# Optimization experiments

Measured on AMD Instinct MI355X. Metric: run time of the kernel, lower is better.

## Reference

```python
import jax, jax.numpy as jnp
import numpy as np

B, S, HID = 2, 2048, 2048
NH, NKV = 16, 4
HD = HID // NH  # 128
GROUPS = NH // NKV


def _rope(x, cos, sin):
    # x: [B, S, H, D]; cos/sin: [S, D//2]
    xr = x.reshape(*x.shape[:-1], HD // 2, 2)
    x0, x1 = xr[..., 0], xr[..., 1]
    c = cos[None, :, None, :]
    s = sin[None, :, None, :]
    o0 = x0 * c - x1 * s
    o1 = x0 * s + x1 * c
    return jnp.stack([o0, o1], axis=-1).reshape(*x.shape)


def setup_inputs() -> dict:
    key = jax.random.key(0)
    k1, k2, k3, k4, k5, k6 = jax.random.split(key, 6)
    hidden_states = jax.random.normal(k1, (B, S, HID), dtype=jnp.float32)
    # RoPE frequencies (llama-style)
    inv_freq = 1.0 / (10000.0 ** (np.arange(0, HD, 2, dtype=np.float32) / HD))
    t = np.arange(S, dtype=np.float32)
    ang = np.outer(t, inv_freq)  # [S, HD//2]
    freqs_cos = jnp.asarray(np.cos(ang), dtype=jnp.float32)
    freqs_sin = jnp.asarray(np.sin(ang), dtype=jnp.float32)
    # additive causal mask [1,1,S,S]
    causal = jnp.triu(jnp.full((S, S), -1e9, dtype=jnp.float32), k=1)
    attention_mask = causal[None, None]
    sc = 0.02
    Wq = jax.random.normal(k2, (NH * HD, HID), dtype=jnp.float32) * sc
    Wk = jax.random.normal(k3, (NKV * HD, HID), dtype=jnp.float32) * sc
    Wv = jax.random.normal(k4, (NKV * HD, HID), dtype=jnp.float32) * sc
    Wo = jax.random.normal(k5, (HID, NH * HD), dtype=jnp.float32) * sc
    return {"hidden_states": hidden_states, "freqs_cos": freqs_cos,
            "freqs_sin": freqs_sin, "attention_mask": attention_mask,
            "Wq": Wq, "Wk": Wk, "Wv": Wv, "Wo": Wo}


def reference(hidden_states, freqs_cos, freqs_sin, attention_mask, Wq, Wk, Wv, Wo):
    xq = (hidden_states @ Wq.T).reshape(B, S, NH, HD)
    xk = (hidden_states @ Wk.T).reshape(B, S, NKV, HD)
    xv = (hidden_states @ Wv.T).reshape(B, S, NKV, HD)
    xq = _rope(xq, freqs_cos, freqs_sin)
    xk = _rope(xk, freqs_cos, freqs_sin)
    # expand KV heads for GQA: [B,S,NKV,D] -> [B,S,NH,D]
    xk = jnp.repeat(xk, GROUPS, axis=2)
    xv = jnp.repeat(xv, GROUPS, axis=2)
    q = xq.transpose(0, 2, 1, 3)  # [B,H,S,D]
    k = xk.transpose(0, 2, 1, 3)
    v = xv.transpose(0, 2, 1, 3)
    scores = jnp.einsum('bhqd,bhkd->bhqk', q, k) / jnp.sqrt(jnp.float32(HD))
    scores = scores + attention_mask
    probs = jax.nn.softmax(scores, axis=-1)
    out = jnp.einsum('bhqk,bhkd->bhqd', probs, v)
    out = out.transpose(0, 2, 1, 3).reshape(B, S, NH * HD)
    return out @ Wo.T
```

## Files before the change

kernel.cpp:

```cpp
#include <hip/hip_runtime.h>


typedef __attribute__((ext_vector_type(8))) short bf16x8;
typedef __attribute__((ext_vector_type(4))) float f32x4;
typedef __attribute__((ext_vector_type(16))) float f32x16;
typedef __attribute__((ext_vector_type(4))) unsigned short u16x4;
typedef unsigned short u16;

#define B_   2
#define S_   2048
#define HID_ 2048
#define NH_  16
#define NKV_ 4
#define HD_  128

__device__ __forceinline__ u16 f2bf(float f) {
  unsigned u = __float_as_uint(f);
  u = (u + 0x7FFFu + ((u >> 16) & 1u)) >> 16;
  return (u16)u;
}
__device__ __forceinline__ float bf2f(u16 h) {
  return __uint_as_float(((unsigned)h) << 16);
}

__device__ __forceinline__ void gl_lds16(const void* g, void* l) {
  __builtin_amdgcn_global_load_lds(
      (const __attribute__((address_space(1))) void*)g,
      (__attribute__((address_space(3))) void*)l, 16, 0, 0);
}

__global__ void convert_bf16(const float* __restrict__ src, u16* __restrict__ dst, int n8) {
  int i = blockIdx.x * 256 + threadIdx.x;
  if (i >= n8) return;
  const float4* s = (const float4*)src + (size_t)i * 2;
  float4 a = s[0], b = s[1];
  union { u16 u[8]; uint4 v; } o;
  o.u[0] = f2bf(a.x); o.u[1] = f2bf(a.y); o.u[2] = f2bf(a.z); o.u[3] = f2bf(a.w);
  o.u[4] = f2bf(b.x); o.u[5] = f2bf(b.y); o.u[6] = f2bf(b.z); o.u[7] = f2bf(b.w);
  ((uint4*)dst)[i] = o.v;
}

template<int EPI>
__launch_bounds__(256, 2)
__global__ void gemm128(const u16* __restrict__ A, const u16* __restrict__ Bm,
                        float* __restrict__ C, u16* __restrict__ Qb,
                        u16* __restrict__ Kb, u16* __restrict__ Vb,
                        int N, int K)
{
  __shared__ u16 As[128 * 64];
  __shared__ u16 Bs[128 * 64];
  const int tid = threadIdx.x;
  const int lane = tid & 63;
  const int w = tid >> 6;
  const int lo = lane & 15, hi = lane >> 4;
  const int wr = w >> 1, wc = w & 1;
  const int rowA0 = blockIdx.x * 128;
  const int rowB0 = blockIdx.y * 128;

  f32x4 acc[4][4] = {};

  for (int kt = 0; kt < K; kt += 64) {
    __syncthreads();
#pragma unroll
    for (int it = 0; it < 4; ++it) {
      int c = it * 256 + tid;
      int r = c >> 3;
      int cb = (c & 7) * 8;
      gl_lds16(A + (size_t)(rowA0 + r) * K + kt + cb, (char*)As + c * 16);
      gl_lds16(Bm + (size_t)(rowB0 + r) * K + kt + cb, (char*)Bs + c * 16);
    }
    __syncthreads();
#pragma unroll
    for (int kk = 0; kk < 64; kk += 32) {
      bf16x8 af[4], bfr[4];
#pragma unroll
      for (int m = 0; m < 4; ++m)
        af[m] = *(const bf16x8*)(As + (wr * 64 + m * 16 + lo) * 64 + kk + hi * 8);
#pragma unroll
      for (int n = 0; n < 4; ++n)
        bfr[n] = *(const bf16x8*)(Bs + (wc * 64 + n * 16 + lo) * 64 + kk + hi * 8);
#pragma unroll
      for (int m = 0; m < 4; ++m)
#pragma unroll
        for (int n = 0; n < 4; ++n)
          acc[m][n] = __builtin_amdgcn_mfma_f32_16x16x32_bf16(af[m], bfr[n], acc[m][n], 0, 0, 0);
    }
  }

#pragma unroll
  for (int m = 0; m < 4; ++m) {
#pragma unroll
    for (int n = 0; n < 4; ++n) {
#pragma unroll
      for (int r = 0; r < 4; ++r) {
        int grow = rowA0 + wr * 64 + m * 16 + hi * 4 + r;
        int gcol = rowB0 + wc * 64 + n * 16 + lo;
        float v = acc[m][n][r];
        if (EPI == 0) {
          C[(size_t)grow * N + gcol] = v;
        } else {
          int bb = grow >> 11, s = grow & 2047;
          u16 hv = f2bf(v);
          if (gcol < 2048) {
            int h = gcol >> 7, d = gcol & 127;
            Qb[(((size_t)bb * NH_ + h) * S_ + s) * HD_ + d] = hv;
          } else if (gcol < 2560) {
            int h = (gcol - 2048) >> 7, d = gcol & 127;
            Kb[(((size_t)bb * NKV_ + h) * S_ + s) * HD_ + d] = hv;
          } else {
            int h = (gcol - 2560) >> 7, d = gcol & 127;
            Vb[(((size_t)bb * NKV_ + h) * S_ + s) * HD_ + d] = hv;
          }
        }
      }
    }
  }
}

__global__ void rope_k(u16* __restrict__ Qb, u16* __restrict__ Kb,
                       const float* __restrict__ fcos, const float* __restrict__ fsin)
{
  int idx = blockIdx.x * 256 + threadIdx.x;
  int chunk = idx & 15;
  int s = (idx >> 4) & 2047;
  int hs = idx >> 15;
  u16* p = (hs < 32) ? (Qb + ((size_t)hs * S_ + s) * HD_ + chunk * 8)
                     : (Kb + ((size_t)(hs - 32) * S_ + s) * HD_ + chunk * 8);
  uint4 raw = *(uint4*)p;
  float4 c4 = *(const float4*)(fcos + (size_t)s * 64 + chunk * 4);
  float4 s4 = *(const float4*)(fsin + (size_t)s * 64 + chunk * 4);
  float cc[4] = {c4.x, c4.y, c4.z, c4.w};
  float ss[4] = {s4.x, s4.y, s4.z, s4.w};
  unsigned* rw = (unsigned*)&raw;
#pragma unroll
  for (int j = 0; j < 4; ++j) {
    float x0 = bf2f((u16)(rw[j] & 0xFFFFu));
    float x1 = bf2f((u16)(rw[j] >> 16));
    float o0 = x0 * cc[j] - x1 * ss[j];
    float o1 = x0 * ss[j] + x1 * cc[j];
    rw[j] = (unsigned)f2bf(o0) | ((unsigned)f2bf(o1) << 16);
  }
  *(uint4*)p = raw;
}

__global__ void transpose_v(const u16* __restrict__ Vb, u16* __restrict__ Vtg)
{
  __shared__ u16 t[64][65];
  const int st = blockIdx.x, dt = blockIdx.y, hs = blockIdx.z;
  const u16* src = Vb + ((size_t)hs * S_ + st * 64) * HD_ + dt * 64;
#pragma unroll
  for (int it = 0; it < 2; ++it) {
    int c = it * 256 + threadIdx.x;
    int r = c >> 3, cb = (c & 7) * 8;
    uint4 v = *(const uint4*)(src + (size_t)r * HD_ + cb);
    u16* u = (u16*)&v;
#pragma unroll
    for (int e = 0; e < 8; ++e) t[r][cb + e] = u[e];
  }
  __syncthreads();
#pragma unroll
  for (int it = 0; it < 2; ++it) {
    int c = it * 256 + threadIdx.x;
    int r2 = c >> 3, cb2 = (c & 7) * 8;
    union { u16 u[8]; uint4 v; } o;
#pragma unroll
    for (int e = 0; e < 8; ++e) o.u[e] = t[cb2 + e][r2];
    *(uint4*)(Vtg + ((size_t)hs * HD_ + dt * 64 + r2) * S_ + st * 64 + cb2) = o.v;
  }
}

__launch_bounds__(128, 2)
__global__ void flash_attn(const u16* __restrict__ Qb, const u16* __restrict__ Kb,
                           const u16* __restrict__ Vtg, u16* __restrict__ AO)
{
  __shared__ u16 Ks[2][64 * 128];
  __shared__ u16 Vt[2][128 * 64];

  const int tid = threadIdx.x, lane = tid & 63, w = tid >> 6;
  const int ql = lane & 31, hh = lane >> 5;
  const int swl = (ql & 7) ^ ((ql >> 3) & 3);
  const int h = blockIdx.y, b = blockIdx.z, kvh = h >> 2;
  const u16* Qh = Qb + ((size_t)b * NH_ + h) * S_ * HD_;
  const u16* Kh = Kb + ((size_t)b * NKV_ + kvh) * S_ * HD_;
  const u16* Vh = Vtg + ((size_t)b * NKV_ + kvh) * HD_ * S_;
  const float cf = 0.12752704581383682f;
  const float NEG = -30000.f;

  auto STAGE = [&](int buf, int kt) {
#pragma unroll
    for (int it = 0; it < 8; ++it) {
      int c = it * 128 + tid;
      int r = c >> 4;
      int slot = (c & 15) ^ (r & 7) ^ ((r >> 3) & 3);
      gl_lds16(Kh + (size_t)(kt + r) * HD_ + slot * 8, (char*)Ks[buf] + c * 16);
    }
#pragma unroll
    for (int it = 0; it < 8; ++it) {
      int c = it * 128 + tid;
      int r = c >> 3;
      int slot = (c & 7) ^ ((r & 7) ^ ((r >> 3) & 3));
      gl_lds16(Vh + (size_t)r * S_ + kt + slot * 8, (char*)Vt[buf] + c * 16);
    }
  };

  for (int pass = 0; pass < 2; ++pass) {
    const int qb = pass ? (31 - (int)blockIdx.x) : (int)blockIdx.x;
    const int q0w = qb * 64 + w * 32;
    const int qg = q0w + ql;
    const int nt = qb + 1;

    bf16x8 qf[8];
#pragma unroll
    for (int s = 0; s < 8; ++s)
      qf[s] = *(const bf16x8*)(Qh + (size_t)qg * HD_ + s * 16 + hh * 8);

    f32x16 o[4] = {};
    float m = NEG, l = 0.f;

    __syncthreads();
    STAGE(0, 0);
    __syncthreads();
    int cur = 0;

    for (int t = 0; t < nt; ++t) {
      if (t < nt - 1) STAGE(cur ^ 1, (t + 1) * 64);
      const int kt = t * 64;
      if (kt < q0w + 32) {
        f32x16 st[2] = {};
        __builtin_amdgcn_s_setprio(1);
#pragma unroll
        for (int sl = 0; sl < 8; ++sl) {
          int slot = ((2 * sl + hh) ^ swl) * 16;
          bf16x8 k0 = *(const bf16x8*)((const char*)Ks[cur] + ql * 256 + slot);
          bf16x8 k1 = *(const bf16x8*)((const char*)Ks[cur] + (32 + ql) * 256 + slot);
          st[0] = __builtin_amdgcn_mfma_f32_32x32x16_bf16(k0, qf[sl], st[0], 0, 0, 0);
          st[1] = __builtin_amdgcn_mfma_f32_32x32x16_bf16(k1, qf[sl], st[1], 0, 0, 0);
        }
        __builtin_amdgcn_s_setprio(0);

        if ((kt + 63) > q0w) {
#pragma unroll
          for (int i = 0; i < 2; ++i)
#pragma unroll
            for (int r = 0; r < 16; ++r) {
              int kv = kt + 32 * i + (r & 3) + 8 * (r >> 2) + 4 * hh;
              if (kv > qg) st[i][r] = NEG;
            }
        }

        float mx[8];
#pragma unroll
        for (int r = 0; r < 8; ++r)
          mx[r] = fmaxf(fmaxf(st[0][r], st[0][r + 8]), fmaxf(st[1][r], st[1][r + 8]));
#pragma unroll
        for (int d = 4; d > 0; d >>= 1)
#pragma unroll
          for (int r = 0; r < d; ++r) mx[r] = fmaxf(mx[r], mx[r + d]);
        float tmax = fmaxf(mx[0], __shfl_xor(mx[0], 32));

        float mn = fmaxf(m, tmax);
        float rs = __builtin_exp2f((m - mn) * cf);
        m = mn; l *= rs;
#pragma unroll
        for (int dt = 0; dt < 4; ++dt)
#pragma unroll
          for (int r = 0; r < 16; ++r) o[dt][r] *= rs;

        const float mc = m * cf;
#pragma unroll
        for (int i = 0; i < 2; ++i)
#pragma unroll
          for (int r = 0; r < 16; ++r)
            st[i][r] = __builtin_exp2f(__builtin_fmaf(st[i][r], cf, -mc));
        float sm[8];
#pragma unroll
        for (int r = 0; r < 8; ++r)
          sm[r] = (st[0][r] + st[0][r + 8]) + (st[1][r] + st[1][r + 8]);
#pragma unroll
        for (int d = 4; d > 0; d >>= 1)
#pragma unroll
          for (int r = 0; r < d; ++r) sm[r] += sm[r + d];
        l += sm[0] + __shfl_xor(sm[0], 32);

        bf16x8 pb[4];
#pragma unroll
        for (int i = 0; i < 2; ++i)
#pragma unroll
          for (int s = 0; s < 2; ++s) {
            unsigned wA, wC, wB, wD;
            asm("v_cvt_pk_bf16_f32 %0, %1, %2" : "=v"(wA) : "v"(st[i][8*s+0]), "v"(st[i][8*s+1]));
            asm("v_cvt_pk_bf16_f32 %0, %1, %2" : "=v"(wC) : "v"(st[i][8*s+2]), "v"(st[i][8*s+3]));
            asm("v_cvt_pk_bf16_f32 %0, %1, %2" : "=v"(wB) : "v"(st[i][8*s+4]), "v"(st[i][8*s+5]));
            asm("v_cvt_pk_bf16_f32 %0, %1, %2" : "=v"(wD) : "v"(st[i][8*s+6]), "v"(st[i][8*s+7]));
            unsigned tA = (unsigned)__shfl_xor((int)wA, 32);
            unsigned tB = (unsigned)__shfl_xor((int)wB, 32);
            unsigned tC = (unsigned)__shfl_xor((int)wC, 32);
            unsigned tD = (unsigned)__shfl_xor((int)wD, 32);
            union { unsigned u[4]; bf16x8 v; } pk;
            pk.u[0] = hh ? tB : wA;
            pk.u[1] = hh ? tD : wC;
            pk.u[2] = hh ? wB : tA;
            pk.u[3] = hh ? wD : tC;
            pb[2 * i + s] = pk.v;
          }

        __builtin_amdgcn_s_setprio(1);
#pragma unroll
        for (int dt = 0; dt < 4; ++dt)
#pragma unroll
          for (int ks = 0; ks < 4; ++ks) {
            int row = 32 * dt + ql;
            bf16x8 vf = *(const bf16x8*)((const char*)Vt[cur] + row * 128 +
                                         (((2 * ks + hh) ^ swl) & 7) * 16);
            o[dt] = __builtin_amdgcn_mfma_f32_32x32x16_bf16(vf, pb[ks], o[dt], 0, 0, 0);
          }
        __builtin_amdgcn_s_setprio(0);
      }
      __syncthreads();
      cur ^= 1;
    }

    const float inv = 1.f / l;
#pragma unroll
    for (int dt = 0; dt < 4; ++dt)
#pragma unroll
      for (int g = 0; g < 4; ++g) {
        u16x4 pk4;
#pragma unroll
        for (int e = 0; e < 4; ++e) pk4[e] = f2bf(o[dt][4 * g + e] * inv);
        *(u16x4*)(AO + ((size_t)b * S_ + qg) * HID_ + h * HD_ + 32 * dt + 8 * g + 4 * hh) = pk4;
      }
  }
}

extern "C" void kernel_launch(void* const* d_in, const int* in_sizes, int n_in,
                              void* d_out, int out_size, void* d_ws, size_t ws_size,
                              hipStream_t stream)
{
  (void)in_sizes; (void)n_in; (void)out_size; (void)ws_size;
  const float* X  = (const float*)d_in[0];
  const float* fc = (const float*)d_in[1];
  const float* fs = (const float*)d_in[2];
  const float* Wq = (const float*)d_in[4];
  const float* Wk = (const float*)d_in[5];
  const float* Wv = (const float*)d_in[6];
  const float* Wo = (const float*)d_in[7];
  float* out = (float*)d_out;

  u16* Xb  = (u16*)d_ws;
  u16* Wb  = Xb + (size_t)4096 * 2048;
  u16* Qb  = Wb + (size_t)3072 * 2048;
  u16* Kb  = Qb + (size_t)B_ * NH_ * S_ * HD_;
  u16* Vb  = Kb + (size_t)B_ * NKV_ * S_ * HD_;
  u16* AO  = Xb;
  u16* Wob = Wb;
  u16* Vtg = Wb + (size_t)2048 * 2048;

  convert_bf16<<<4096, 256, 0, stream>>>(X,  Xb,               4096 * 2048 / 8);
  convert_bf16<<<2048, 256, 0, stream>>>(Wq, Wb,               2048 * 2048 / 8);
  convert_bf16<<<512,  256, 0, stream>>>(Wk, Wb + 2048 * 2048, 512 * 2048 / 8);
  convert_bf16<<<512,  256, 0, stream>>>(Wv, Wb + 2560 * 2048, 512 * 2048 / 8);

  gemm128<1><<<dim3(32, 24), 256, 0, stream>>>(Xb, Wb, nullptr, Qb, Kb, Vb, 3072, 2048);

  convert_bf16<<<2048, 256, 0, stream>>>(Wo, Wob, 2048 * 2048 / 8);

  transpose_v<<<dim3(32, 2, 8), 256, 0, stream>>>(Vb, Vtg);

  rope_k<<<5120, 256, 0, stream>>>(Qb, Kb, fc, fs);

  flash_attn<<<dim3(16, NH_, B_), 128, 0, stream>>>(Qb, Kb, Vtg, AO);

  gemm128<0><<<dim3(32, 16), 256, 0, stream>>>(AO, Wob, out, nullptr, nullptr, nullptr, 2048, 2048);
}
```

Before: 240.2 us.

## Drop LDS staging in flash attention; waves load K/V directly from global

Flash attention no longer uses double-buffered shared-memory tiles and barriers. Each of four waves per block takes its own 32-row query tile, chosen so causal work balances across waves, and loads K and V fragments straight from global memory into registers before the MFMAs. A lazy rescale skips the accumulator correction when the running max grows by only a small amount. This removes LDS traffic and block syncs at the cost of redundant global/L2 loads of K and V across waves, and more register pressure.

```diff
diff --git a/kernel.cpp b/kernel.cpp
--- a/kernel.cpp
+++ b/kernel.cpp
@@ -169,168 +169,144 @@
   }
 }
 
-__launch_bounds__(128, 2)
+__launch_bounds__(256, 2)
 __global__ void flash_attn(const u16* __restrict__ Qb, const u16* __restrict__ Kb,
                            const u16* __restrict__ Vtg, u16* __restrict__ AO)
 {
-  __shared__ u16 Ks[2][64 * 128];
-  __shared__ u16 Vt[2][128 * 64];
-
   const int tid = threadIdx.x, lane = tid & 63, w = tid >> 6;
   const int ql = lane & 31, hh = lane >> 5;
-  const int swl = (ql & 7) ^ ((ql >> 3) & 3);
-  const int h = blockIdx.y, b = blockIdx.z, kvh = h >> 2;
+  const int x = blockIdx.x, h = blockIdx.y, b = blockIdx.z, kvh = h >> 2;
   const u16* Qh = Qb + ((size_t)b * NH_ + h) * S_ * HD_;
   const u16* Kh = Kb + ((size_t)b * NKV_ + kvh) * S_ * HD_;
   const u16* Vh = Vtg + ((size_t)b * NKV_ + kvh) * HD_ * S_;
   const float cf = 0.12752704581383682f;
   const float NEG = -30000.f;
 
-  auto STAGE = [&](int buf, int kt) {
-#pragma unroll
-    for (int it = 0; it < 8; ++it) {
-      int c = it * 128 + tid;
-      int r = c >> 4;
-      int slot = (c & 15) ^ (r & 7) ^ ((r >> 3) & 3);
-      gl_lds16(Kh + (size_t)(kt + r) * HD_ + slot * 8, (char*)Ks[buf] + c * 16);
-    }
-#pragma unroll
-    for (int it = 0; it < 8; ++it) {
-      int c = it * 128 + tid;
-      int r = c >> 3;
-      int slot = (c & 7) ^ ((r & 7) ^ ((r >> 3) & 3));
-      gl_lds16(Vh + (size_t)r * S_ + kt + slot * 8, (char*)Vt[buf] + c * 16);
-    }
-  };
-
-  for (int pass = 0; pass < 2; ++pass) {
-    const int qb = pass ? (31 - (int)blockIdx.x) : (int)blockIdx.x;
-    const int q0w = qb * 64 + w * 32;
-    const int qg = q0w + ql;
-    const int nt = qb + 1;
-
-    bf16x8 qf[8];
-#pragma unroll
-    for (int s = 0; s < 8; ++s)
-      qf[s] = *(const bf16x8*)(Qh + (size_t)qg * HD_ + s * 16 + hh * 8);
-
-    f32x16 o[4] = {};
-    float m = NEG, l = 0.f;
-
-    __syncthreads();
-    STAGE(0, 0);
-    __syncthreads();
-    int cur = 0;
-
-    for (int t = 0; t < nt; ++t) {
-      if (t < nt - 1) STAGE(cur ^ 1, (t + 1) * 64);
-      const int kt = t * 64;
-      if (kt < q0w + 32) {
-        f32x16 st[2] = {};
-        __builtin_amdgcn_s_setprio(1);
-#pragma unroll
-        for (int sl = 0; sl < 8; ++sl) {
-          int slot = ((2 * sl + hh) ^ swl) * 16;
-          bf16x8 k0 = *(const bf16x8*)((const char*)Ks[cur] + ql * 256 + slot);
-          bf16x8 k1 = *(const bf16x8*)((const char*)Ks[cur] + (32 + ql) * 256 + slot);
-          st[0] = __builtin_amdgcn_mfma_f32_32x32x16_bf16(k0, qf[sl], st[0], 0, 0, 0);
-          st[1] = __builtin_amdgcn_mfma_f32_32x32x16_bf16(k1, qf[sl], st[1], 0, 0, 0);
+  const int qt = (w == 0) ? x : (w == 1) ? (63 - x) : (w == 2) ? (31 - x) : (32 + x);
+  const int q0 = qt * 32;
+  const int qg = q0 + ql;
+  const int nt = (qt >> 1) + 1;
+
+  bf16x8 qf[8];
+#pragma unroll
+  for (int s = 0; s < 8; ++s)
+    qf[s] = *(const bf16x8*)(Qh + (size_t)qg * HD_ + s * 16 + hh * 8);
+
+  f32x16 o[4] = {};
+  float m = NEG, l = 0.f;
+
+  for (int t = 0; t < nt; ++t) {
+    const int kt = t * 64;
+    const u16* Kt = Kh + (size_t)kt * HD_;
+
+    bf16x8 k0[8], k1[8];
+#pragma unroll
+    for (int sl = 0; sl < 8; ++sl)
+      k0[sl] = *(const bf16x8*)(Kt + (size_t)ql * HD_ + sl * 16 + hh * 8);
+#pragma unroll
+    for (int sl = 0; sl < 8; ++sl)
+      k1[sl] = *(const bf16x8*)(Kt + (size_t)(32 + ql) * HD_ + sl * 16 + hh * 8);
+    f32x16 st[2] = {};
+    __builtin_amdgcn_s_setprio(1);
+#pragma unroll
+    for (int sl = 0; sl < 8; ++sl) {
+      st[0] = __builtin_amdgcn_mfma_f32_32x32x16_bf16(k0[sl], qf[sl], st[0], 0, 0, 0);
+      st[1] = __builtin_amdgcn_mfma_f32_32x32x16_bf16(k1[sl], qf[sl], st[1], 0, 0, 0);
+    }
+    __builtin_amdgcn_s_setprio(0);
+
+    if (kt + 63 > q0) {
+#pragma unroll
+      for (int i = 0; i < 2; ++i)
+#pragma unroll
+        for (int r = 0; r < 16; ++r) {
+          int kv = kt + 32 * i + (r & 3) + 8 * (r >> 2) + 4 * hh;
+          if (kv > qg) st[i][r] = NEG;
         }
-        __builtin_amdgcn_s_setprio(0);
-
-        if ((kt + 63) > q0w) {
-#pragma unroll
-          for (int i = 0; i < 2; ++i)
-#pragma unroll
-            for (int r = 0; r < 16; ++r) {
-              int kv = kt + 32 * i + (r & 3) + 8 * (r >> 2) + 4 * hh;
-              if (kv > qg) st[i][r] = NEG;
-            }
-        }
-
-        float mx[8];
-#pragma unroll
-        for (int r = 0; r < 8; ++r)
-          mx[r] = fmaxf(fmaxf(st[0][r], st[0][r + 8]), fmaxf(st[1][r], st[1][r + 8]));
-#pragma unroll
-        for (int d = 4; d > 0; d >>= 1)
-#pragma unroll
-          for (int r = 0; r < d; ++r) mx[r] = fmaxf(mx[r], mx[r + d]);
-        float tmax = fmaxf(mx[0], __shfl_xor(mx[0], 32));
-
-        float mn = fmaxf(m, tmax);
-        float rs = __builtin_exp2f((m - mn) * cf);
-        m = mn; l *= rs;
-#pragma unroll
-        for (int dt = 0; dt < 4; ++dt)
-#pragma unroll
-          for (int r = 0; r < 16; ++r) o[dt][r] *= rs;
-
-        const float mc = m * cf;
-#pragma unroll
-        for (int i = 0; i < 2; ++i)
-#pragma unroll
-          for (int r = 0; r < 16; ++r)
-            st[i][r] = __builtin_exp2f(__builtin_fmaf(st[i][r], cf, -mc));
-        float sm[8];
-#pragma unroll
-        for (int r = 0; r < 8; ++r)
-          sm[r] = (st[0][r] + st[0][r + 8]) + (st[1][r] + st[1][r + 8]);
-#pragma unroll
-        for (int d = 4; d > 0; d >>= 1)
-#pragma unroll
-          for (int r = 0; r < d; ++r) sm[r] += sm[r + d];
-        l += sm[0] + __shfl_xor(sm[0], 32);
-
-        bf16x8 pb[4];
-#pragma unroll
-        for (int i = 0; i < 2; ++i)
-#pragma unroll
-          for (int s = 0; s < 2; ++s) {
-            unsigned wA, wC, wB, wD;
-            asm("v_cvt_pk_bf16_f32 %0, %1, %2" : "=v"(wA) : "v"(st[i][8*s+0]), "v"(st[i][8*s+1]));
-            asm("v_cvt_pk_bf16_f32 %0, %1, %2" : "=v"(wC) : "v"(st[i][8*s+2]), "v"(st[i][8*s+3]));
-            asm("v_cvt_pk_bf16_f32 %0, %1, %2" : "=v"(wB) : "v"(st[i][8*s+4]), "v"(st[i][8*s+5]));
-            asm("v_cvt_pk_bf16_f32 %0, %1, %2" : "=v"(wD) : "v"(st[i][8*s+6]), "v"(st[i][8*s+7]));
-            unsigned tA = (unsigned)__shfl_xor((int)wA, 32);
-            unsigned tB = (unsigned)__shfl_xor((int)wB, 32);
-            unsigned tC = (unsigned)__shfl_xor((int)wC, 32);
-            unsigned tD = (unsigned)__shfl_xor((int)wD, 32);
-            union { unsigned u[4]; bf16x8 v; } pk;
-            pk.u[0] = hh ? tB : wA;
-            pk.u[1] = hh ? tD : wC;
-            pk.u[2] = hh ? wB : tA;
-            pk.u[3] = hh ? wD : tC;
-            pb[2 * i + s] = pk.v;
-          }
-
-        __builtin_amdgcn_s_setprio(1);
-#pragma unroll
-        for (int dt = 0; dt < 4; ++dt)
-#pragma unroll
-          for (int ks = 0; ks < 4; ++ks) {
-            int row = 32 * dt + ql;
-            bf16x8 vf = *(const bf16x8*)((const char*)Vt[cur] + row * 128 +
-                                         (((2 * ks + hh) ^ swl) & 7) * 16);
-            o[dt] = __builtin_amdgcn_mfma_f32_32x32x16_bf16(vf, pb[ks], o[dt], 0, 0, 0);
-          }
-        __builtin_amdgcn_s_setprio(0);
+    }
+
+    float mx[8];
+#pragma unroll
+    for (int r = 0; r < 8; ++r)
+      mx[r] = fmaxf(fmaxf(st[0][r], st[0][r + 8]), fmaxf(st[1][r], st[1][r + 8]));
+#pragma unroll
+    for (int d = 4; d > 0; d >>= 1)
+#pragma unroll
+      for (int r = 0; r < d; ++r) mx[r] = fmaxf(mx[r], mx[r + d]);
+    float tmax = fmaxf(mx[0], __shfl_xor(mx[0], 32));
+
+    if (!__all((tmax - m) * cf <= 8.f)) {
+      float mn = fmaxf(m, tmax);
+      float rs = __builtin_exp2f((m - mn) * cf);
+      m = mn; l *= rs;
+#pragma unroll
+      for (int dt = 0; dt < 4; ++dt)
+#pragma unroll
+        for (int r = 0; r < 16; ++r) o[dt][r] *= rs;
+    }
+
+    const float mc = m * cf;
+#pragma unroll
+    for (int i = 0; i < 2; ++i)
+#pragma unroll
+      for (int r = 0; r < 16; ++r)
+        st[i][r] = __builtin_exp2f(__builtin_fmaf(st[i][r], cf, -mc));
+    float sm[8];
+#pragma unroll
+    for (int r = 0; r < 8; ++r)
+      sm[r] = (st[0][r] + st[0][r + 8]) + (st[1][r] + st[1][r + 8]);
+#pragma unroll
+    for (int d = 4; d > 0; d >>= 1)
+#pragma unroll
+      for (int r = 0; r < d; ++r) sm[r] += sm[r + d];
+    l += sm[0] + __shfl_xor(sm[0], 32);
+
+    bf16x8 pb[4];
+#pragma unroll
+    for (int i = 0; i < 2; ++i)
+#pragma unroll
+      for (int s = 0; s < 2; ++s) {
+        unsigned wA, wC, wB, wD;
+        asm("v_cvt_pk_bf16_f32 %0, %1, %2" : "=v"(wA) : "v"(st[i][8*s+0]), "v"(st[i][8*s+1]));
+        asm("v_cvt_pk_bf16_f32 %0, %1, %2" : "=v"(wC) : "v"(st[i][8*s+2]), "v"(st[i][8*s+3]));
+        asm("v_cvt_pk_bf16_f32 %0, %1, %2" : "=v"(wB) : "v"(st[i][8*s+4]), "v"(st[i][8*s+5]));
+        asm("v_cvt_pk_bf16_f32 %0, %1, %2" : "=v"(wD) : "v"(st[i][8*s+6]), "v"(st[i][8*s+7]));
+        unsigned tA = (unsigned)__shfl_xor((int)wA, 32);
+        unsigned tB = (unsigned)__shfl_xor((int)wB, 32);
+        unsigned tC = (unsigned)__shfl_xor((int)wC, 32);
+        unsigned tD = (unsigned)__shfl_xor((int)wD, 32);
+        union { unsigned u[4]; bf16x8 v; } pk;
+        pk.u[0] = hh ? tB : wA;
+        pk.u[1] = hh ? tD : wC;
+        pk.u[2] = hh ? wB : tA;
+        pk.u[3] = hh ? wD : tC;
+        pb[2 * i + s] = pk.v;
       }
-      __syncthreads();
-      cur ^= 1;
-    }
-
-    const float inv = 1.f / l;
-#pragma unroll
-    for (int dt = 0; dt < 4; ++dt)
-#pragma unroll
-      for (int g = 0; g < 4; ++g) {
-        u16x4 pk4;
-#pragma unroll
-        for (int e = 0; e < 4; ++e) pk4[e] = f2bf(o[dt][4 * g + e] * inv);
-        *(u16x4*)(AO + ((size_t)b * S_ + qg) * HID_ + h * HD_ + 32 * dt + 8 * g + 4 * hh) = pk4;
-      }
-  }
+
+#pragma unroll
+    for (int dt = 0; dt < 4; ++dt) {
+      bf16x8 vf[4];
+#pragma unroll
+      for (int ks = 0; ks < 4; ++ks)
+        vf[ks] = *(const bf16x8*)(Vh + (size_t)(32 * dt + ql) * S_ + kt + ks * 16 + hh * 8);
+      __builtin_amdgcn_s_setprio(1);
+#pragma unroll
+      for (int ks = 0; ks < 4; ++ks)
+        o[dt] = __builtin_amdgcn_mfma_f32_32x32x16_bf16(vf[ks], pb[ks], o[dt], 0, 0, 0);
+      __builtin_amdgcn_s_setprio(0);
+    }
+  }
+
+  const float inv = 1.f / l;
+#pragma unroll
+  for (int dt = 0; dt < 4; ++dt)
+#pragma unroll
+    for (int g = 0; g < 4; ++g) {
+      u16x4 pk4;
+#pragma unroll
+      for (int e = 0; e < 4; ++e) pk4[e] = f2bf(o[dt][4 * g + e] * inv);
+      *(u16x4*)(AO + ((size_t)b * S_ + qg) * HID_ + h * HD_ + 32 * dt + 8 * g + 4 * hh) = pk4;
+    }
 }
 
 extern "C" void kernel_launch(void* const* d_in, const int* in_sizes, int n_in,
@@ -369,7 +345,7 @@
 
   rope_k<<<5120, 256, 0, stream>>>(Qb, Kb, fc, fs);
 
-  flash_attn<<<dim3(16, NH_, B_), 128, 0, stream>>>(Qb, Kb, Vtg, AO);
+  flash_attn<<<dim3(16, NH_, B_), 256, 0, stream>>>(Qb, Kb, Vtg, AO);
 
   gemm128<0><<<dim3(32, 16), 256, 0, stream>>>(AO, Wob, out, nullptr, nullptr, nullptr, 2048, 2048);
 }
```

Measured after the change: 289.8 us. 20.6% more time.

## Restructure flash attention into 4-wave blocks with balanced causal tiles and lazy rescale

Applied to the files above, without the earlier changes.

Replaces the two-pass, two-wave flash attention block with a single-pass, four-wave block. Each wave takes a 32-row query tile chosen from a complementary set (x, 63-x, 31-x, 32+x), so each block carries a similar amount of causal work and one staged K/V pipeline is shared by more waves. The grid is flattened, and the block index is mapped so that blocks sharing a KV head and batch sit close together, which should help L2 reuse. It also adds a lazy softmax rescale that skips the max update and the accumulator rescale while the new maximum stays within a bounded exponent, trading fewer VALU multiplies for extra range reliance on fp32 accumulation.

```diff
diff --git a/kernel.cpp b/kernel.cpp
--- a/kernel.cpp
+++ b/kernel.cpp
@@ -169,7 +169,7 @@
   }
 }
 
-__launch_bounds__(128, 2)
+__launch_bounds__(256, 2)
 __global__ void flash_attn(const u16* __restrict__ Qb, const u16* __restrict__ Kb,
                            const u16* __restrict__ Vtg, u16* __restrict__ AO)
 {
@@ -179,85 +179,90 @@
   const int tid = threadIdx.x, lane = tid & 63, w = tid >> 6;
   const int ql = lane & 31, hh = lane >> 5;
   const int swl = (ql & 7) ^ ((ql >> 3) & 3);
-  const int h = blockIdx.y, b = blockIdx.z, kvh = h >> 2;
+
+  const int lin = blockIdx.x;
+  const int g = lin & 7, idx = lin >> 3;
+  const int b = g >> 2, kvh = g & 3;
+  const int h = kvh * 4 + (idx >> 4);
+  const int x = idx & 15;
+
   const u16* Qh = Qb + ((size_t)b * NH_ + h) * S_ * HD_;
   const u16* Kh = Kb + ((size_t)b * NKV_ + kvh) * S_ * HD_;
   const u16* Vh = Vtg + ((size_t)b * NKV_ + kvh) * HD_ * S_;
   const float cf = 0.12752704581383682f;
   const float NEG = -30000.f;
 
+  const int qt = (w == 0) ? x : (w == 1) ? (63 - x) : (w == 2) ? (31 - x) : (32 + x);
+  const int q0 = qt * 32;
+  const int qg = q0 + ql;
+  const int bnt = ((63 - x) >> 1) + 1;
+
   auto STAGE = [&](int buf, int kt) {
 #pragma unroll
-    for (int it = 0; it < 8; ++it) {
-      int c = it * 128 + tid;
+    for (int it = 0; it < 4; ++it) {
+      int c = it * 256 + tid;
       int r = c >> 4;
       int slot = (c & 15) ^ (r & 7) ^ ((r >> 3) & 3);
       gl_lds16(Kh + (size_t)(kt + r) * HD_ + slot * 8, (char*)Ks[buf] + c * 16);
     }
 #pragma unroll
-    for (int it = 0; it < 8; ++it) {
-      int c = it * 128 + tid;
+    for (int it = 0; it < 4; ++it) {
+      int c = it * 256 + tid;
       int r = c >> 3;
       int slot = (c & 7) ^ ((r & 7) ^ ((r >> 3) & 3));
       gl_lds16(Vh + (size_t)r * S_ + kt + slot * 8, (char*)Vt[buf] + c * 16);
     }
   };
 
-  for (int pass = 0; pass < 2; ++pass) {
-    const int qb = pass ? (31 - (int)blockIdx.x) : (int)blockIdx.x;
-    const int q0w = qb * 64 + w * 32;
-    const int qg = q0w + ql;
-    const int nt = qb + 1;
-
-    bf16x8 qf[8];
-#pragma unroll
-    for (int s = 0; s < 8; ++s)
-      qf[s] = *(const bf16x8*)(Qh + (size_t)qg * HD_ + s * 16 + hh * 8);
-
-    f32x16 o[4] = {};
-    float m = NEG, l = 0.f;
-
-    __syncthreads();
-    STAGE(0, 0);
-    __syncthreads();
-    int cur = 0;
-
-    for (int t = 0; t < nt; ++t) {
-      if (t < nt - 1) STAGE(cur ^ 1, (t + 1) * 64);
-      const int kt = t * 64;
-      if (kt < q0w + 32) {
-        f32x16 st[2] = {};
-        __builtin_amdgcn_s_setprio(1);
-#pragma unroll
-        for (int sl = 0; sl < 8; ++sl) {
-          int slot = ((2 * sl + hh) ^ swl) * 16;
-          bf16x8 k0 = *(const bf16x8*)((const char*)Ks[cur] + ql * 256 + slot);
-          bf16x8 k1 = *(const bf16x8*)((const char*)Ks[cur] + (32 + ql) * 256 + slot);
-          st[0] = __builtin_amdgcn_mfma_f32_32x32x16_bf16(k0, qf[sl], st[0], 0, 0, 0);
-          st[1] = __builtin_amdgcn_mfma_f32_32x32x16_bf16(k1, qf[sl], st[1], 0, 0, 0);
-        }
-        __builtin_amdgcn_s_setprio(0);
-
-        if ((kt + 63) > q0w) {
-#pragma unroll
-          for (int i = 0; i < 2; ++i)
-#pragma unroll
-            for (int r = 0; r < 16; ++r) {
-              int kv = kt + 32 * i + (r & 3) + 8 * (r >> 2) + 4 * hh;
-              if (kv > qg) st[i][r] = NEG;
-            }
-        }
-
-        float mx[8];
-#pragma unroll
-        for (int r = 0; r < 8; ++r)
-          mx[r] = fmaxf(fmaxf(st[0][r], st[0][r + 8]), fmaxf(st[1][r], st[1][r + 8]));
-#pragma unroll
-        for (int d = 4; d > 0; d >>= 1)
-#pragma unroll
-          for (int r = 0; r < d; ++r) mx[r] = fmaxf(mx[r], mx[r + d]);
-        float tmax = fmaxf(mx[0], __shfl_xor(mx[0], 32));
-
+  bf16x8 qf[8];
+#pragma unroll
+  for (int s = 0; s < 8; ++s)
+    qf[s] = *(const bf16x8*)(Qh + (size_t)qg * HD_ + s * 16 + hh * 8);
+
+  f32x16 o[4] = {};
+  float m = NEG, l = 0.f;
+
+  STAGE(0, 0);
+  __syncthreads();
+  int cur = 0;
+
+  for (int t = 0; t < bnt; ++t) {
+    if (t + 1 < bnt) STAGE(cur ^ 1, (t + 1) * 64);
+    const int kt = t * 64;
+    if (kt < q0 + 32) {
+      f32x16 st[2] = {};
+      __builtin_amdgcn_s_setprio(1);
+#pragma unroll
+      for (int sl = 0; sl < 8; ++sl) {
+        int slot = ((2 * sl + hh) ^ swl) * 16;
+        bf16x8 k0 = *(const bf16x8*)((const char*)Ks[cur] + ql * 256 + slot);
+        bf16x8 k1 = *(const bf16x8*)((const char*)Ks[cur] + (32 + ql) * 256 + slot);
+        st[0] = __builtin_amdgcn_mfma_f32_32x32x16_bf16(k0, qf[sl], st[0], 0, 0, 0);
+        st[1] = __builtin_amdgcn_mfma_f32_32x32x16_bf16(k1, qf[sl], st[1], 0, 0, 0);
+      }
+      __builtin_amdgcn_s_setprio(0);
+
+      if ((kt + 63) > q0) {
+#pragma unroll
+        for (int i = 0; i < 2; ++i)
+#pragma unroll
+          for (int r = 0; r < 16; ++r) {
+            int kv = kt + 32 * i + (r & 3) + 8 * (r >> 2) + 4 * hh;
+            if (kv > qg) st[i][r] = NEG;
+          }
+      }
+
+      float mx[8];
+#pragma unroll
+      for (int r = 0; r < 8; ++r)
+        mx[r] = fmaxf(fmaxf(st[0][r], st[0][r + 8]), fmaxf(st[1][r], st[1][r + 8]));
+#pragma unroll
+      for (int d = 4; d > 0; d >>= 1)
+#pragma unroll
+        for (int r = 0; r < d; ++r) mx[r] = fmaxf(mx[r], mx[r + d]);
+      float tmax = fmaxf(mx[0], __shfl_xor(mx[0], 32));
+
+      if (!__all((tmax - m) * cf <= 8.f)) {
         float mn = fmaxf(m, tmax);
         float rs = __builtin_exp2f((m - mn) * cf);
         m = mn; l *= rs;
@@ -265,72 +270,72 @@
         for (int dt = 0; dt < 4; ++dt)
 #pragma unroll
           for (int r = 0; r < 16; ++r) o[dt][r] *= rs;
-
-        const float mc = m * cf;
-#pragma unroll
-        for (int i = 0; i < 2; ++i)
-#pragma unroll
-          for (int r = 0; r < 16; ++r)
-            st[i][r] = __builtin_exp2f(__builtin_fmaf(st[i][r], cf, -mc));
-        float sm[8];
-#pragma unroll
-        for (int r = 0; r < 8; ++r)
-          sm[r] = (st[0][r] + st[0][r + 8]) + (st[1][r] + st[1][r + 8]);
-#pragma unroll
-        for (int d = 4; d > 0; d >>= 1)
-#pragma unroll
-          for (int r = 0; r < d; ++r) sm[r] += sm[r + d];
-        l += sm[0] + __shfl_xor(sm[0], 32);
-
-        bf16x8 pb[4];
-#pragma unroll
-        for (int i = 0; i < 2; ++i)
-#pragma unroll
-          for (int s = 0; s < 2; ++s) {
-            unsigned wA, wC, wB, wD;
-            asm("v_cvt_pk_bf16_f32 %0, %1, %2" : "=v"(wA) : "v"(st[i][8*s+0]), "v"(st[i][8*s+1]));
-            asm("v_cvt_pk_bf16_f32 %0, %1, %2" : "=v"(wC) : "v"(st[i][8*s+2]), "v"(st[i][8*s+3]));
-            asm("v_cvt_pk_bf16_f32 %0, %1, %2" : "=v"(wB) : "v"(st[i][8*s+4]), "v"(st[i][8*s+5]));
-            asm("v_cvt_pk_bf16_f32 %0, %1, %2" : "=v"(wD) : "v"(st[i][8*s+6]), "v"(st[i][8*s+7]));
-            unsigned tA = (unsigned)__shfl_xor((int)wA, 32);
-            unsigned tB = (unsigned)__shfl_xor((int)wB, 32);
-            unsigned tC = (unsigned)__shfl_xor((int)wC, 32);
-            unsigned tD = (unsigned)__shfl_xor((int)wD, 32);
-            union { unsigned u[4]; bf16x8 v; } pk;
-            pk.u[0] = hh ? tB : wA;
-            pk.u[1] = hh ? tD : wC;
-            pk.u[2] = hh ? wB : tA;
-            pk.u[3] = hh ? wD : tC;
-            pb[2 * i + s] = pk.v;
-          }
-
-        __builtin_amdgcn_s_setprio(1);
-#pragma unroll
-        for (int dt = 0; dt < 4; ++dt)
-#pragma unroll
-          for (int ks = 0; ks < 4; ++ks) {
-            int row = 32 * dt + ql;
-            bf16x8 vf = *(const bf16x8*)((const char*)Vt[cur] + row * 128 +
-                                         (((2 * ks + hh) ^ swl) & 7) * 16);
-            o[dt] = __builtin_amdgcn_mfma_f32_32x32x16_bf16(vf, pb[ks], o[dt], 0, 0, 0);
-          }
-        __builtin_amdgcn_s_setprio(0);
       }
-      __syncthreads();
-      cur ^= 1;
-    }
-
-    const float inv = 1.f / l;
-#pragma unroll
-    for (int dt = 0; dt < 4; ++dt)
-#pragma unroll
-      for (int g = 0; g < 4; ++g) {
-        u16x4 pk4;
-#pragma unroll
-        for (int e = 0; e < 4; ++e) pk4[e] = f2bf(o[dt][4 * g + e] * inv);
-        *(u16x4*)(AO + ((size_t)b * S_ + qg) * HID_ + h * HD_ + 32 * dt + 8 * g + 4 * hh) = pk4;
-      }
-  }
+
+      const float mc = m * cf;
+#pragma unroll
+      for (int i = 0; i < 2; ++i)
+#pragma unroll
+        for (int r = 0; r < 16; ++r)
+          st[i][r] = __builtin_exp2f(__builtin_fmaf(st[i][r], cf, -mc));
+      float sm[8];
+#pragma unroll
+      for (int r = 0; r < 8; ++r)
+        sm[r] = (st[0][r] + st[0][r + 8]) + (st[1][r] + st[1][r + 8]);
+#pragma unroll
+      for (int d = 4; d > 0; d >>= 1)
+#pragma unroll
+        for (int r = 0; r < d; ++r) sm[r] += sm[r + d];
+      l += sm[0] + __shfl_xor(sm[0], 32);
+
+      bf16x8 pb[4];
+#pragma unroll
+      for (int i = 0; i < 2; ++i)
+#pragma unroll
+        for (int s = 0; s < 2; ++s) {
+          unsigned wA, wC, wB, wD;
+          asm("v_cvt_pk_bf16_f32 %0, %1, %2" : "=v"(wA) : "v"(st[i][8*s+0]), "v"(st[i][8*s+1]));
+          asm("v_cvt_pk_bf16_f32 %0, %1, %2" : "=v"(wC) : "v"(st[i][8*s+2]), "v"(st[i][8*s+3]));
+          asm("v_cvt_pk_bf16_f32 %0, %1, %2" : "=v"(wB) : "v"(st[i][8*s+4]), "v"(st[i][8*s+5]));
+          asm("v_cvt_pk_bf16_f32 %0, %1, %2" : "=v"(wD) : "v"(st[i][8*s+6]), "v"(st[i][8*s+7]));
+          unsigned tA = (unsigned)__shfl_xor((int)wA, 32);
+          unsigned tB = (unsigned)__shfl_xor((int)wB, 32);
+          unsigned tC = (unsigned)__shfl_xor((int)wC, 32);
+          unsigned tD = (unsigned)__shfl_xor((int)wD, 32);
+          union { unsigned u[4]; bf16x8 v; } pk;
+          pk.u[0] = hh ? tB : wA;
+          pk.u[1] = hh ? tD : wC;
+          pk.u[2] = hh ? wB : tA;
+          pk.u[3] = hh ? wD : tC;
+          pb[2 * i + s] = pk.v;
+        }
+
+      __builtin_amdgcn_s_setprio(1);
+#pragma unroll
+      for (int dt = 0; dt < 4; ++dt)
+#pragma unroll
+        for (int ks = 0; ks < 4; ++ks) {
+          int row = 32 * dt + ql;
+          bf16x8 vf = *(const bf16x8*)((const char*)Vt[cur] + row * 128 +
+                                       (((2 * ks + hh) ^ swl) & 7) * 16);
+          o[dt] = __builtin_amdgcn_mfma_f32_32x32x16_bf16(vf, pb[ks], o[dt], 0, 0, 0);
+        }
+      __builtin_amdgcn_s_setprio(0);
+    }
+    __syncthreads();
+    cur ^= 1;
+  }
+
+  const float inv = 1.f / l;
+#pragma unroll
+  for (int dt = 0; dt < 4; ++dt)
+#pragma unroll
+    for (int gi = 0; gi < 4; ++gi) {
+      u16x4 pk4;
+#pragma unroll
+      for (int e = 0; e < 4; ++e) pk4[e] = f2bf(o[dt][4 * gi + e] * inv);
+      *(u16x4*)(AO + ((size_t)b * S_ + qg) * HID_ + h * HD_ + 32 * dt + 8 * gi + 4 * hh) = pk4;
+    }
 }
 
 extern "C" void kernel_launch(void* const* d_in, const int* in_sizes, int n_in,
@@ -369,7 +374,7 @@
 
   rope_k<<<5120, 256, 0, stream>>>(Qb, Kb, fc, fs);
 
-  flash_attn<<<dim3(16, NH_, B_), 128, 0, stream>>>(Qb, Kb, Vtg, AO);
+  flash_attn<<<512, 256, 0, stream>>>(Qb, Kb, Vtg, AO);
 
   gemm128<0><<<dim3(32, 16), 256, 0, stream>>>(AO, Wob, out, nullptr, nullptr, nullptr, 2048, 2048);
 }
```

Result: faster. 233.5 us (-2.8%).
